# Kernel optimization log

Measured on AMD Instinct MI355X. Metric: run time of the kernel, lower is better.

Reference implementation:

```python
import jax, jax.numpy as jnp
import numpy as np

N, E, G = 100000, 1600000, 64
IN, H, OUT = 128, 64, 16  # hidden/2 = 32
SLOPE = 0.01


def setup_inputs() -> dict:
    key = jax.random.key(0)
    ks = jax.random.split(key, 7)
    features = jax.random.normal(ks[0], (N, IN), dtype=jnp.float32)
    src = jax.random.randint(ks[1], (E,), 0, N)
    dst = jax.random.randint(ks[2], (E,), 0, N)
    graph_ids = jnp.sort(jax.random.randint(ks[3], (N,), 0, G))
    # kaiming-uniform-ish fan_in init, bias=False everywhere
    W1 = jax.random.uniform(ks[4], (IN, H), jnp.float32, -1.0, 1.0) * np.sqrt(3.0 / IN)
    W2 = jax.random.uniform(ks[5], (H, H // 2), jnp.float32, -1.0, 1.0) * np.sqrt(3.0 / H)
    Wc = jax.random.uniform(ks[6], (H // 2, OUT), jnp.float32, -1.0, 1.0) * np.sqrt(3.0 / (H // 2))
    return {"features": features, "src": src, "dst": dst, "graph_ids": graph_ids,
            "W1": W1, "W2": W2, "Wc": Wc}


def _graph_conv(x, W, src, dst, n):
    # DGL GraphConv, norm='both', bias=False:
    # out = D_in^{-1/2} A (D_out^{-1/2} x) W   (degrees clamped to >= 1)
    ones = jnp.ones(src.shape[0], dtype=x.dtype)
    outdeg = jnp.clip(jax.ops.segment_sum(ones, src, num_segments=n), 1.0)
    indeg = jnp.clip(jax.ops.segment_sum(ones, dst, num_segments=n), 1.0)
    h = (x * jax.lax.rsqrt(outdeg)[:, None]) @ W  # project first (in_dim > out_dim)
    m = jax.ops.segment_sum(h[src], dst, num_segments=n)  # sparse aggregation
    return m * jax.lax.rsqrt(indeg)[:, None]


def reference(features, src, dst, graph_ids, W1, W2, Wc):
    h = jax.nn.leaky_relu(_graph_conv(features, W1, src, dst, N), SLOPE)
    h = jax.nn.leaky_relu(_graph_conv(h, W2, src, dst, N), SLOPE)
    # dropout is identity at inference
    sums = jax.ops.segment_sum(h, graph_ids, num_segments=G)
    cnts = jnp.clip(jax.ops.segment_sum(jnp.ones((N,), h.dtype), graph_ids, num_segments=G), 1.0)
    mean = sums / cnts[:, None]  # dgl.mean_nodes
    return mean @ Wc  # [G, OUT]
```

## Files before the change

kernel.cpp:

```cpp
#include <hip/hip_runtime.h>

#define NN 100000
#define NE 1600000
#define NG 64
#define D_IN 128
#define D_H 64
#define D_H2 32
#define D_OUT 16
#define SLOPE 0.01f
#define REC 48

#define BSH 9
#define NBK 196
#define NCB 500
#define CHE (NE / NCB)
#define PCAP 56

typedef _Float16 half2v __attribute__((ext_vector_type(2)));
typedef _Float16 h8 __attribute__((ext_vector_type(8)));
typedef float f32x4 __attribute__((ext_vector_type(4)));

__global__ __launch_bounds__(512) void p12_scatter(const int* __restrict__ src,
                                                   const int* __restrict__ dst,
                                                   unsigned* __restrict__ pkD,
                                                   unsigned short* __restrict__ pkS,
                                                   int* __restrict__ cntD,
                                                   int* __restrict__ cntS,
                                                   float* __restrict__ pool) {
  __shared__ int cD[NBK], cS[NBK];
  int b = blockIdx.x, t = threadIdx.x;
  if (b == 0) {
    for (int i = t; i < NG * D_H2; i += 512) pool[i] = 0.f;
  }
  for (int i = t; i < NBK; i += 512) { cD[i] = 0; cS[i] = 0; }
  __syncthreads();
  const int4* s4 = (const int4*)(src + b * CHE);
  const int4* d4 = (const int4*)(dst + b * CHE);
  for (int i = t; i < CHE / 4; i += 512) {
    int4 s = s4[i], d = d4[i];
#pragma unroll
    for (int j = 0; j < 4; ++j) {
      int ss = (j == 0) ? s.x : (j == 1) ? s.y : (j == 2) ? s.z : s.w;
      int dd = (j == 0) ? d.x : (j == 1) ? d.y : (j == 2) ? d.z : d.w;
      int kd = dd >> BSH;
      int pd = atomicAdd(&cD[kd], 1);
      if (pd < PCAP) pkD[((size_t)kd * NCB + b) * PCAP + pd] =
          ((unsigned)(dd & 511) << 17) | (unsigned)ss;
      int ks = ss >> BSH;
      int ps = atomicAdd(&cS[ks], 1);
      if (ps < PCAP) pkS[((size_t)ks * NCB + b) * PCAP + ps] =
          (unsigned short)(ss & 511);
    }
  }
  __syncthreads();
  for (int i = t; i < NBK; i += 512) {
    cntD[i * NCB + b] = min(cD[i], PCAP);
    cntS[i * NCB + b] = min(cS[i], PCAP);
  }
}

__global__ __launch_bounds__(512) void p3_build(const unsigned* __restrict__ pkD,
                                                const unsigned short* __restrict__ pkS,
                                                const int* __restrict__ cntD,
                                                const int* __restrict__ cntS,
                                                int* __restrict__ adj,
                                                int* __restrict__ indeg,
                                                int* __restrict__ outdeg) {
  __shared__ int hh[512];
  int bb = blockIdx.x, t = threadIdx.x;
  hh[t] = 0;
  __syncthreads();
  if (bb < NBK) {
    int k = bb;
    int n0 = k << BSH;
    if (t < NCB) {
      int cnt = cntD[k * NCB + t];
      const uint4* r4 = (const uint4*)(pkD + ((size_t)k * NCB + t) * PCAP);
      for (int i = 0; i * 4 < cnt; ++i) {
        uint4 v = r4[i];
#pragma unroll
        for (int j = 0; j < 4; ++j) {
          int idx = i * 4 + j;
          if (idx < cnt) {
            unsigned rec = (j == 0) ? v.x : (j == 1) ? v.y : (j == 2) ? v.z : v.w;
            int local = rec >> 17;
            int pos = atomicAdd(&hh[local], 1);
            if (pos < REC) adj[(size_t)(n0 + local) * REC + pos] = (int)(rec & 0x1FFFF);
          }
        }
      }
    }
    __syncthreads();
    int4 ph = make_int4(NN, NN, NN, NN);
    {
      int n = n0 + t;
      if (n < NN) {
        int dg = hh[t];
        indeg[n] = dg;
        int d = min(dg, REC);
        int dr = min((d + 15) & ~15, REC);
        int j = d;
        for (; j & 3; ++j) if (j < dr) adj[(size_t)n * REC + j] = NN;
        for (; j + 4 <= dr; j += 4) *(int4*)&adj[(size_t)n * REC + j] = ph;
      }
    }
  } else {
    int k = bb - NBK;
    if (t < NCB) {
      int cnt = cntS[k * NCB + t];
      const uint4* r4 = (const uint4*)(pkS + ((size_t)k * NCB + t) * PCAP);
      for (int i = 0; i * 8 < cnt; ++i) {
        uint4 v = r4[i];
        const unsigned short* u = (const unsigned short*)&v;
#pragma unroll
        for (int j = 0; j < 8; ++j) {
          int idx = i * 8 + j;
          if (idx < cnt) atomicAdd(&hh[u[j]], 1);
        }
      }
    }
    __syncthreads();
    int n0 = k << BSH;
    int n = n0 + t;
    if (n < NN) outdeg[n] = hh[t];
  }
}

__global__ __launch_bounds__(256) void k_mm1f(const float* __restrict__ X,
                                              const float* __restrict__ W,
                                              const int* __restrict__ odeg,
                                              _Float16* __restrict__ Y) {
  __shared__ _Float16 Wt[64][136];
  int t = threadIdx.x;
  if (blockIdx.x == 0 && t < 64) Y[(size_t)NN * 64 + t] = (_Float16)0.f;
  for (int i = t; i < 128 * 64; i += 256) {
    int k = i >> 6, f = i & 63;
    Wt[f][k] = (_Float16)W[i];
  }
  __syncthreads();
  int lane = t & 63, w = t >> 6;
  int m = lane & 15, q = lane >> 4;
  h8 bf[4][4];
#pragma unroll
  for (int kc = 0; kc < 4; ++kc)
#pragma unroll
    for (int nt = 0; nt < 4; ++nt)
      bf[kc][nt] = *(const h8*)&Wt[nt * 16 + m][kc * 32 + q * 8];

  const int NT = NN / 16;
  int idx = blockIdx.x * 4 + w;
  int t0 = idx * 2, t1 = t0 + 1;
  f32x4 r0[8], r1[8];
  if (t0 < NT) {
    const f32x4* X0 = (const f32x4*)(X + (size_t)(t0 * 16 + m) * 128);
#pragma unroll
    for (int kc = 0; kc < 4; ++kc) {
      r0[kc * 2 + 0] = X0[kc * 8 + q * 2 + 0];
      r0[kc * 2 + 1] = X0[kc * 8 + q * 2 + 1];
    }
  }
  if (t1 < NT) {
    const f32x4* X1 = (const f32x4*)(X + (size_t)(t1 * 16 + m) * 128);
#pragma unroll
    for (int kc = 0; kc < 4; ++kc) {
      r1[kc * 2 + 0] = X1[kc * 8 + q * 2 + 0];
      r1[kc * 2 + 1] = X1[kc * 8 + q * 2 + 1];
    }
  }
#pragma unroll
  for (int half = 0; half < 2; ++half) {
    int tile = (half == 0) ? t0 : t1;
    if (tile >= NT) continue;
    f32x4* rr = (half == 0) ? r0 : r1;
    f32x4 acc[4] = {{0,0,0,0},{0,0,0,0},{0,0,0,0},{0,0,0,0}};
#pragma unroll
    for (int kc = 0; kc < 4; ++kc) {
      f32x4 x0 = rr[kc * 2 + 0], x1 = rr[kc * 2 + 1];
      h8 a;
      a[0] = (_Float16)x0.x; a[1] = (_Float16)x0.y;
      a[2] = (_Float16)x0.z; a[3] = (_Float16)x0.w;
      a[4] = (_Float16)x1.x; a[5] = (_Float16)x1.y;
      a[6] = (_Float16)x1.z; a[7] = (_Float16)x1.w;
#pragma unroll
      for (int nt = 0; nt < 4; ++nt)
        acc[nt] = __builtin_amdgcn_mfma_f32_16x16x32_f16(a, bf[kc][nt], acc[nt], 0, 0, 0);
    }
    int n0 = tile * 16;
#pragma unroll
    for (int reg = 0; reg < 4; ++reg) {
      int nn = n0 + q * 4 + reg;
      float sc = rsqrtf((float)max(odeg[nn], 1));
#pragma unroll
      for (int nt = 0; nt < 4; ++nt)
        Y[(size_t)nn * 64 + nt * 16 + m] = (_Float16)(acc[nt][reg] * sc);
    }
  }
}

__global__ __launch_bounds__(256)
__attribute__((amdgpu_waves_per_eu(4)))
void k_aggmm2(const int* __restrict__ adj,
              const int* __restrict__ indeg,
              const int* __restrict__ odeg,
              const h8* __restrict__ H8,
              const float* __restrict__ W,
              _Float16* __restrict__ Y) {
  __shared__ int Adj[32][REC];
  __shared__ int Deg[32];
  __shared__ _Float16 Ht[32][72];
  __shared__ _Float16 Wt[32][72];
  int t = threadIdx.x;
  if (blockIdx.x == 0 && t < 32) Y[(size_t)NN * 32 + t] = (_Float16)0.f;
  for (int i = t; i < 64 * 32; i += 256) {
    int k = i >> 5, f = i & 31;
    Wt[f][k] = (_Float16)W[i];
  }
  int node0 = blockIdx.x * 32;
  {
    const int4* gadj = (const int4*)(adj + (size_t)node0 * REC);
    for (int i = t; i < 32 * (REC / 4); i += 256)
      ((int4*)Adj)[i] = gadj[i];
    if (t < 32) Deg[t] = indeg[node0 + t];
  }
  __syncthreads();
  int l8 = t & 7;
  int nd = t >> 3;
  int deg = Deg[nd];
  int groups = (min(deg, REC) + 15) >> 4;
  float acc[8] = {0.f, 0.f, 0.f, 0.f, 0.f, 0.f, 0.f, 0.f};
  for (int g = 0; g < groups; ++g) {
    int4 c0 = *(const int4*)&Adj[nd][g * 16 + 0];
    int4 c1 = *(const int4*)&Adj[nd][g * 16 + 4];
    int4 c2 = *(const int4*)&Adj[nd][g * 16 + 8];
    int4 c3 = *(const int4*)&Adj[nd][g * 16 + 12];
    h8 v0 = H8[(size_t)c0.x * 8 + l8];
    h8 v1 = H8[(size_t)c0.y * 8 + l8];
    h8 v2 = H8[(size_t)c0.z * 8 + l8];
    h8 v3 = H8[(size_t)c0.w * 8 + l8];
    h8 v4 = H8[(size_t)c1.x * 8 + l8];
    h8 v5 = H8[(size_t)c1.y * 8 + l8];
    h8 v6 = H8[(size_t)c1.z * 8 + l8];
    h8 v7 = H8[(size_t)c1.w * 8 + l8];
    h8 v8 = H8[(size_t)c2.x * 8 + l8];
    h8 v9 = H8[(size_t)c2.y * 8 + l8];
    h8 va = H8[(size_t)c2.z * 8 + l8];
    h8 vb = H8[(size_t)c2.w * 8 + l8];
    h8 vc = H8[(size_t)c3.x * 8 + l8];
    h8 vd = H8[(size_t)c3.y * 8 + l8];
    h8 ve = H8[(size_t)c3.z * 8 + l8];
    h8 vf = H8[(size_t)c3.w * 8 + l8];
#pragma unroll
    for (int j = 0; j < 8; ++j)
      acc[j] += ((((float)v0[j] + (float)v1[j]) + ((float)v2[j] + (float)v3[j])) +
                 (((float)v4[j] + (float)v5[j]) + ((float)v6[j] + (float)v7[j]))) +
                ((((float)v8[j] + (float)v9[j]) + ((float)va[j] + (float)vb[j])) +
                 (((float)vc[j] + (float)vd[j]) + ((float)ve[j] + (float)vf[j])));
  }
  float sc = rsqrtf((float)max(deg, 1));
  h8 hv;
#pragma unroll
  for (int j = 0; j < 8; ++j) {
    float x = acc[j] * sc;
    hv[j] = (_Float16)((x > 0.f) ? x : SLOPE * x);
  }
  *(h8*)&Ht[nd][l8 * 8] = hv;
  __syncthreads();
  int lane = t & 63, w = t >> 6;
  if (w < 2) {
    int m = lane & 15, q = lane >> 4;
    h8 bf[2][2];
#pragma unroll
    for (int kc = 0; kc < 2; ++kc)
#pragma unroll
      for (int nt = 0; nt < 2; ++nt)
        bf[kc][nt] = *(const h8*)&Wt[nt * 16 + m][kc * 32 + q * 8];
    h8 af[2];
#pragma unroll
    for (int kc = 0; kc < 2; ++kc)
      af[kc] = *(const h8*)&Ht[w * 16 + m][kc * 32 + q * 8];
    f32x4 acc2[2] = {{0, 0, 0, 0}, {0, 0, 0, 0}};
#pragma unroll
    for (int kc = 0; kc < 2; ++kc)
#pragma unroll
      for (int nt = 0; nt < 2; ++nt)
        acc2[nt] = __builtin_amdgcn_mfma_f32_16x16x32_f16(af[kc], bf[kc][nt], acc2[nt], 0, 0, 0);
#pragma unroll
    for (int reg = 0; reg < 4; ++reg) {
      int nn = blockIdx.x * 32 + w * 16 + q * 4 + reg;
      float sco = rsqrtf((float)max(odeg[nn], 1));
#pragma unroll
      for (int nt = 0; nt < 2; ++nt)
        Y[(size_t)nn * 32 + nt * 16 + m] = (_Float16)(acc2[nt][reg] * sco);
    }
  }
}

__global__ __launch_bounds__(256)
__attribute__((amdgpu_waves_per_eu(4)))
void k_agg32p(const int* __restrict__ adj,
              const int* __restrict__ indeg,
              const int* __restrict__ gid,
              const h8* __restrict__ H8,
              float* __restrict__ pool) {
  __shared__ int Adj2[64][REC];
  __shared__ int Deg2[64];
  __shared__ float lp[4][D_H2];
  __shared__ int gmin_s;
  int t = threadIdx.x;
  int l4 = t & 3;
  int nd = t >> 2;
  int node0 = blockIdx.x * 64;
  int node = node0 + nd;
  bool valid = node < NN;
  if (t == 0) gmin_s = gid[node0];
  for (int i = t; i < 4 * D_H2; i += 256) ((float*)lp)[i] = 0.f;
  {
    int maxi = (min(NN - node0, 64)) * (REC / 4);
    const int4* gadj = (const int4*)(adj + (size_t)node0 * REC);
    for (int i = t; i < 64 * (REC / 4); i += 256)
      ((int4*)Adj2)[i] = (i < maxi) ? gadj[i] : make_int4(NN, NN, NN, NN);
    if (t < 64) Deg2[t] = (node0 + t < NN) ? indeg[node0 + t] : 0;
  }
  __syncthreads();
  int deg = Deg2[nd];
  int groups = (min(deg, REC) + 15) >> 4;
  float acc[8] = {0.f, 0.f, 0.f, 0.f, 0.f, 0.f, 0.f, 0.f};
  for (int g = 0; g < groups; ++g) {
    int4 c0 = *(const int4*)&Adj2[nd][g * 16 + 0];
    int4 c1 = *(const int4*)&Adj2[nd][g * 16 + 4];
    int4 c2 = *(const int4*)&Adj2[nd][g * 16 + 8];
    int4 c3 = *(const int4*)&Adj2[nd][g * 16 + 12];
    h8 v0 = H8[(size_t)c0.x * 4 + l4];
    h8 v1 = H8[(size_t)c0.y * 4 + l4];
    h8 v2 = H8[(size_t)c0.z * 4 + l4];
    h8 v3 = H8[(size_t)c0.w * 4 + l4];
    h8 v4 = H8[(size_t)c1.x * 4 + l4];
    h8 v5 = H8[(size_t)c1.y * 4 + l4];
    h8 v6 = H8[(size_t)c1.z * 4 + l4];
    h8 v7 = H8[(size_t)c1.w * 4 + l4];
    h8 v8 = H8[(size_t)c2.x * 4 + l4];
    h8 v9 = H8[(size_t)c2.y * 4 + l4];
    h8 va = H8[(size_t)c2.z * 4 + l4];
    h8 vb = H8[(size_t)c2.w * 4 + l4];
    h8 vc = H8[(size_t)c3.x * 4 + l4];
    h8 vd = H8[(size_t)c3.y * 4 + l4];
    h8 ve = H8[(size_t)c3.z * 4 + l4];
    h8 vf = H8[(size_t)c3.w * 4 + l4];
#pragma unroll
    for (int j = 0; j < 8; ++j)
      acc[j] += ((((float)v0[j] + (float)v1[j]) + ((float)v2[j] + (float)v3[j])) +
                 (((float)v4[j] + (float)v5[j]) + ((float)v6[j] + (float)v7[j]))) +
                ((((float)v8[j] + (float)v9[j]) + ((float)va[j] + (float)vb[j])) +
                 (((float)vc[j] + (float)vd[j]) + ((float)ve[j] + (float)vf[j])));
  }
  if (valid) {
    float sc = rsqrtf((float)max(deg, 1));
    int gl = min(gid[node] - gmin_s, 3);
#pragma unroll
    for (int j = 0; j < 8; ++j) {
      float x = acc[j] * sc;
      x = (x > 0.f) ? x : SLOPE * x;
      atomicAdd(&lp[gl][l4 * 8 + j], x);
    }
  }
  __syncthreads();
  if (t < 4 * D_H2) {
    float v = ((float*)lp)[t];
    if (v != 0.f) {
      int gl = t >> 5, f = t & 31;
      atomicAdd(&pool[(gmin_s + gl) * D_H2 + f], v);
    }
  }
}

__global__ __launch_bounds__(256) void k_out(const float* __restrict__ pool,
                                             const int* __restrict__ gid,
                                             const float* __restrict__ Wc,
                                             float* __restrict__ out) {
  __shared__ int bnd[NG + 1];
  __shared__ float mean[NG][D_H2];
  int t = threadIdx.x;
  if (t <= NG) {
    int target = t;
    int lo = 0, hi = NN;
    while (lo < hi) {
      int mid = (lo + hi) >> 1;
      if (gid[mid] < target) lo = mid + 1; else hi = mid;
    }
    bnd[t] = lo;
  }
  __syncthreads();
  for (int i = t; i < NG * D_H2; i += 256) {
    int g = i >> 5;
    float inv = 1.0f / (float)max(bnd[g + 1] - bnd[g], 1);
    ((float*)mean)[i] = pool[i] * inv;
  }
  __syncthreads();
  for (int i = t; i < NG * D_OUT; i += 256) {
    int g = i / D_OUT, o = i % D_OUT;
    float s = 0.f;
#pragma unroll
    for (int c = 0; c < D_H2; ++c) s += mean[g][c] * Wc[c * D_OUT + o];
    out[i] = s;
  }
}

extern "C" void kernel_launch(void* const* d_in, const int* in_sizes, int n_in,
                              void* d_out, int out_size, void* d_ws, size_t ws_size,
                              hipStream_t stream) {
  const float* X  = (const float*)d_in[0];
  const int*   src = (const int*)d_in[1];
  const int*   dst = (const int*)d_in[2];
  const int*   gid = (const int*)d_in[3];
  const float* W1 = (const float*)d_in[4];
  const float* W2 = (const float*)d_in[5];
  const float* Wc = (const float*)d_in[6];
  float* out = (float*)d_out;

  char* p = (char*)d_ws;
  auto alloc = [&](size_t bytes) {
    char* q = p;
    p += (bytes + 255) & ~(size_t)255;
    return q;
  };
  float*          pool   = (float*)alloc(NG * D_H2 * 4);
  int*            outdeg = (int*)alloc(NN * 4);
  int*            indeg  = (int*)alloc(NN * 4);
  int*            cntD   = (int*)alloc((size_t)NBK * NCB * 4);
  int*            cntS   = (int*)alloc((size_t)NBK * NCB * 4);
  unsigned*       pkD    = (unsigned*)alloc((size_t)NBK * NCB * PCAP * 4);
  unsigned short* pkS    = (unsigned short*)alloc((size_t)NBK * NCB * PCAP * 2);
  int*            adj    = (int*)alloc((size_t)NN * REC * 4);
  _Float16*       bufA   = (_Float16*)alloc((size_t)(NN + 1) * 64 * 2);
  _Float16*       bufC   = (_Float16*)alloc((size_t)(NN + 1) * 32 * 2);

  p12_scatter<<<NCB, 512, 0, stream>>>(src, dst, pkD, pkS, cntD, cntS, pool);
  p3_build<<<2 * NBK, 512, 0, stream>>>(pkD, pkS, cntD, cntS, adj, indeg, outdeg);

  k_mm1f<<<782, 256, 0, stream>>>(X, W1, outdeg, bufA);
  k_aggmm2<<<NN / 32, 256, 0, stream>>>(adj, indeg, outdeg, (const h8*)bufA, W2, bufC);
  k_agg32p<<<(NN + 63) / 64, 256, 0, stream>>>(adj, indeg, gid, (const h8*)bufC, pool);
  k_out<<<1, 256, 0, stream>>>(pool, gid, Wc, out);
}
```

Measured before the change: 217.9 us.

## Stage scatter buckets in LDS, move adjacency padding into aggregation kernels

The scatter kernel now gathers per-bucket records in shared memory and writes them out contiguously per wave, replacing scattered global stores. The bucket capacity drops from 56 to 48 so the LDS staging arrays fit. The build kernel no longer writes NN padding into the adjacency rows; each aggregation kernel instead overwrites entries past the degree with NN in shared memory after loading. The waves_per_eu occupancy hints are also removed. The lower capacity raises the chance that overflowing edges in a chunk are silently dropped, and the extra padding pass adds a barrier and integer division in each aggregation block.

```diff
diff --git a/kernel.cpp b/kernel.cpp
--- a/kernel.cpp
+++ b/kernel.cpp
@@ -14,7 +14,7 @@
 #define NBK 196
 #define NCB 500
 #define CHE (NE / NCB)
-#define PCAP 56
+#define PCAP 48
 
 typedef _Float16 half2v __attribute__((ext_vector_type(2)));
 typedef _Float16 h8 __attribute__((ext_vector_type(8)));
@@ -27,6 +27,8 @@
                                                    int* __restrict__ cntD,
                                                    int* __restrict__ cntS,
                                                    float* __restrict__ pool) {
+  __shared__ unsigned stD[NBK][PCAP];
+  __shared__ unsigned short stS[NBK][PCAP];
   __shared__ int cD[NBK], cS[NBK];
   int b = blockIdx.x, t = threadIdx.x;
   if (b == 0) {
@@ -44,15 +46,19 @@
       int dd = (j == 0) ? d.x : (j == 1) ? d.y : (j == 2) ? d.z : d.w;
       int kd = dd >> BSH;
       int pd = atomicAdd(&cD[kd], 1);
-      if (pd < PCAP) pkD[((size_t)kd * NCB + b) * PCAP + pd] =
-          ((unsigned)(dd & 511) << 17) | (unsigned)ss;
+      if (pd < PCAP) stD[kd][pd] = ((unsigned)(dd & 511) << 17) | (unsigned)ss;
       int ks = ss >> BSH;
       int ps = atomicAdd(&cS[ks], 1);
-      if (ps < PCAP) pkS[((size_t)ks * NCB + b) * PCAP + ps] =
-          (unsigned short)(ss & 511);
-    }
-  }
-  __syncthreads();
+      if (ps < PCAP) stS[ks][ps] = (unsigned short)(ss & 511);
+    }
+  }
+  __syncthreads();
+  int wid = t >> 6, lane = t & 63;
+  for (int k = wid; k < NBK; k += 8) {
+    int cd = min(cD[k], PCAP), cs = min(cS[k], PCAP);
+    if (lane < cd) pkD[((size_t)k * NCB + b) * PCAP + lane] = stD[k][lane];
+    if (lane < cs) pkS[((size_t)k * NCB + b) * PCAP + lane] = stS[k][lane];
+  }
   for (int i = t; i < NBK; i += 512) {
     cntD[i * NCB + b] = min(cD[i], PCAP);
     cntS[i * NCB + b] = min(cS[i], PCAP);
@@ -91,19 +97,8 @@
       }
     }
     __syncthreads();
-    int4 ph = make_int4(NN, NN, NN, NN);
-    {
-      int n = n0 + t;
-      if (n < NN) {
-        int dg = hh[t];
-        indeg[n] = dg;
-        int d = min(dg, REC);
-        int dr = min((d + 15) & ~15, REC);
-        int j = d;
-        for (; j & 3; ++j) if (j < dr) adj[(size_t)n * REC + j] = NN;
-        for (; j + 4 <= dr; j += 4) *(int4*)&adj[(size_t)n * REC + j] = ph;
-      }
-    }
+    int n = n0 + t;
+    if (n < NN) indeg[n] = hh[t];
   } else {
     int k = bb - NBK;
     if (t < NCB) {
@@ -198,7 +193,6 @@
 }
 
 __global__ __launch_bounds__(256)
-__attribute__((amdgpu_waves_per_eu(4)))
 void k_aggmm2(const int* __restrict__ adj,
               const int* __restrict__ indeg,
               const int* __restrict__ odeg,
@@ -221,6 +215,11 @@
     for (int i = t; i < 32 * (REC / 4); i += 256)
       ((int4*)Adj)[i] = gadj[i];
     if (t < 32) Deg[t] = indeg[node0 + t];
+  }
+  __syncthreads();
+  for (int i = t; i < 32 * REC; i += 256) {
+    int ndc = i / REC, j = i % REC;
+    if (j >= min(Deg[ndc], REC)) Adj[ndc][j] = NN;
   }
   __syncthreads();
   int l8 = t & 7;
@@ -296,7 +295,6 @@
 }
 
 __global__ __launch_bounds__(256)
-__attribute__((amdgpu_waves_per_eu(4)))
 void k_agg32p(const int* __restrict__ adj,
               const int* __restrict__ indeg,
               const int* __restrict__ gid,
@@ -320,6 +318,11 @@
     for (int i = t; i < 64 * (REC / 4); i += 256)
       ((int4*)Adj2)[i] = (i < maxi) ? gadj[i] : make_int4(NN, NN, NN, NN);
     if (t < 64) Deg2[t] = (node0 + t < NN) ? indeg[node0 + t] : 0;
+  }
+  __syncthreads();
+  for (int i = t; i < 64 * REC; i += 256) {
+    int ndc = i / REC, j = i % REC;
+    if (j >= min(Deg2[ndc], REC)) Adj2[ndc][j] = NN;
   }
   __syncthreads();
   int deg = Deg2[nd];
```

Result: no change. 214.4 us (-1.6%).
